# Performance work log

Hardware: AMD Instinct MI355X
Metric: run time of the kernel (lower is better)

Reference implementation:

```python
import jax, jax.numpy as jnp
import numpy as np

B, N, K, D_MODEL = 4, 16384, 32, 64

def gather_neighbors(x, idx):
    # x: [B, N, F], idx: [B, N, K] -> [B, N, K, F]
    return jnp.take_along_axis(x[:, :, None, :], idx[:, :, :, None], axis=1)

def setup_inputs() -> dict:
    key = jax.random.key(0)
    k1, k2, k3, k4, k5 = jax.random.split(key, 5)
    x = jax.random.normal(k1, (B, N, D_MODEL), dtype=jnp.float32)
    pos = jax.random.normal(k2, (B, N, 3), dtype=jnp.float32)
    neighbor_idx = jax.random.randint(k3, (B, N, K), 0, N, dtype=jnp.int32)
    W1 = jax.random.normal(k4, (3, D_MODEL), dtype=jnp.float32) * (1.0 / np.sqrt(3.0))
    b1 = jnp.zeros((D_MODEL,), dtype=jnp.float32)
    W2 = jax.random.normal(k5, (D_MODEL, D_MODEL), dtype=jnp.float32) * (1.0 / np.sqrt(D_MODEL))
    b2 = jnp.zeros((D_MODEL,), dtype=jnp.float32)
    return {"x": x, "pos": pos, "neighbor_idx": neighbor_idx,
            "W1": W1, "b1": b1, "W2": W2, "b2": b2}

def reference(x, pos, neighbor_idx, W1, b1, W2, b2):
    # gather neighbor positions: [B, N, K, 3]
    neighbors = gather_neighbors(pos, neighbor_idx)
    rel_pos = pos[:, :, None, :] - neighbors              # [B, N, K, 3]
    # weight MLP: Linear(3,d) + LeakyReLU(0.1), Linear(d,d)
    h = jax.nn.leaky_relu(jnp.einsum('bnkd,df->bnkf', rel_pos, W1) + b1, 0.1)
    w = jnp.einsum('bnkf,fg->bnkg', h, W2) + b2           # [B, N, K, F]
    xg = gather_neighbors(x, neighbor_idx)                # [B, N, K, F]
    return jnp.sum(w * xg, axis=2)                        # [B, N, F]
```

## Files before the change

### kernel.cpp

```cpp
#include <hip/hip_runtime.h>


#define NPTS   16384
#define KNB    32
#define F      64
#define BATCH  4
#define LOG2N  14
#define WPTS   8

typedef _Float16 h2     __attribute__((ext_vector_type(2)));
typedef _Float16 h8     __attribute__((ext_vector_type(8)));
typedef float    f32x16 __attribute__((ext_vector_type(16)));

__global__ __launch_bounds__(256, 2) void pointconv_mfma(
    const float* __restrict__ x,
    const float* __restrict__ pos,
    const int*   __restrict__ idx,
    const float* __restrict__ W1,
    const float* __restrict__ b1,
    const float* __restrict__ W2,
    const float* __restrict__ b2,
    float*       __restrict__ out)
{
    __shared__ __align__(16) _Float16 w1p[32][8];
    __shared__ __align__(16) _Float16 w2f[2][4][2][32][8];

    const int tid = threadIdx.x;
    if (tid < 32) {
        const int g = 2 * tid;
        w1p[tid][0] = (_Float16)W1[0 * F + g]; w1p[tid][1] = (_Float16)W1[0 * F + g + 1];
        w1p[tid][2] = (_Float16)W1[1 * F + g]; w1p[tid][3] = (_Float16)W1[1 * F + g + 1];
        w1p[tid][4] = (_Float16)W1[2 * F + g]; w1p[tid][5] = (_Float16)W1[2 * F + g + 1];
        w1p[tid][6] = (_Float16)b1[g];         w1p[tid][7] = (_Float16)b1[g + 1];
    }
#pragma unroll
    for (int r = 0; r < 16; ++r) {
        const int e = r * 256 + tid;
        const int g = e >> 6, f = e & 63;
        w2f[(g >> 3) & 1][g >> 4][f & 1][f >> 1][g & 7] = (_Float16)W2[e];
    }
    __syncthreads();

    const int lane = tid & 63;
    const int wv   = tid >> 6;
    const int m    = lane & 31;
    const int hf   = lane >> 5;
    const int voff = hf << 4;

    const float2 b2v = *(const float2*)(b2 + 2 * m);

    const int p0   = (blockIdx.x * 4 + wv) * WPTS;
    const int p0_s = __builtin_amdgcn_readfirstlane(p0);
    const int base = (p0_s >> LOG2N) << LOG2N;
    const uint32_t m2 = 2u * (uint32_t)m;

    const h2 c01 = { (_Float16)0.1f, (_Float16)0.1f };

    float2 xvA[16], xvB[16];
    float  rlA[6], rlB[6];
    int    jmA = 0, jmB = 0;
    {
        const int jm0 = idx[(uint32_t)(p0_s * KNB) + (uint32_t)m];
#pragma unroll
        for (int reg = 0; reg < 16; ++reg) {
            const int rA = (reg & 3) + ((reg >> 2) << 3);
            const int jk = __builtin_amdgcn_ds_bpermute(voff + 4 * rA, jm0);
            const uint32_t xo = ((uint32_t)(base + jk) << 6) + m2;
            xvA[reg] = *(const float2*)(x + xo);
        }
        const uint32_t nr3 = 3u * (uint32_t)(base + jm0);
        const uint32_t pp3 = 3u * (uint32_t)p0_s;
        rlA[0] = pos[nr3];     rlA[1] = pos[nr3 + 1]; rlA[2] = pos[nr3 + 2];
        rlA[3] = pos[pp3];     rlA[4] = pos[pp3 + 1]; rlA[5] = pos[pp3 + 2];
        if (WPTS > 1) jmA = idx[(uint32_t)((p0_s + 1) * KNB) + (uint32_t)m];
    }

#define POINT_BODY(XV_CUR, XV_NXT, JM_CUR, JM_NXT, RL_CUR, RL_NXT, I)         \
    {                                                                         \
        const int p_s = p0_s + (I);                                           \
         \
        if ((I) + 2 < WPTS)                                                   \
            JM_NXT = idx[(uint32_t)((p_s + 2) * KNB) + (uint32_t)m];          \
           \
        if ((I) + 1 < WPTS) {                                                 \
            const uint32_t nr3 = 3u * (uint32_t)(base + JM_CUR);              \
            const uint32_t pp3 = 3u * (uint32_t)(p_s + 1);                    \
            RL_NXT[0] = pos[nr3];     RL_NXT[1] = pos[nr3 + 1];               \
            RL_NXT[2] = pos[nr3 + 2];                                         \
            RL_NXT[3] = pos[pp3];     RL_NXT[4] = pos[pp3 + 1];               \
            RL_NXT[5] = pos[pp3 + 2];                                         \
        }                                                                     \
          \
        if ((I) + 1 < WPTS) {                                                 \
            _Pragma("unroll")                                                 \
            for (int reg = 0; reg < 16; ++reg) {                              \
                const int rA = (reg & 3) + ((reg >> 2) << 3);                 \
                const int jk = __builtin_amdgcn_ds_bpermute(voff + 4 * rA, JM_CUR); \
                const uint32_t xo = ((uint32_t)(base + jk) << 6) + m2;        \
                XV_NXT[reg] = *(const float2*)(x + xo);                       \
            }                                                                 \
        }                                                                     \
                \
        const float rx = RL_CUR[3] - RL_CUR[0];                               \
        const float ry = RL_CUR[4] - RL_CUR[1];                               \
        const float rz = RL_CUR[5] - RL_CUR[2];                               \
        f32x16 acc0, acc1;                                                    \
        _Pragma("unroll")                                                     \
        for (int r = 0; r < 16; ++r) { acc0[r] = b2v.x; acc1[r] = b2v.y; }    \
        const h2 rxp = { (_Float16)rx, (_Float16)rx };                        \
        const h2 ryp = { (_Float16)ry, (_Float16)ry };                        \
        const h2 rzp = { (_Float16)rz, (_Float16)rz };                        \
        _Pragma("unroll")                                                     \
        for (int t = 0; t < 4; ++t) {                                         \
            h8 af;                                                            \
            _Pragma("unroll")                                                 \
            for (int jj = 0; jj < 4; ++jj) {                                  \
                const int g2 = 8 * t + 4 * hf + jj;                           \
                const h8 w = *(const h8*)&w1p[g2][0];                         \
                const h2 wx = __builtin_shufflevector(w, w, 0, 1);            \
                const h2 wy = __builtin_shufflevector(w, w, 2, 3);            \
                const h2 wz = __builtin_shufflevector(w, w, 4, 5);            \
                const h2 bb = __builtin_shufflevector(w, w, 6, 7);            \
                h2 hv = bb + rxp * wx;                                        \
                hv = hv + ryp * wy;                                           \
                hv = hv + rzp * wz;                                           \
                hv = __builtin_elementwise_max(hv, hv * c01);                 \
                af[2 * jj]     = hv[0];                                       \
                af[2 * jj + 1] = hv[1];                                       \
            }                                                                 \
            const h8 bf0 = *(const h8*)&w2f[hf][t][0][m][0];                  \
            const h8 bf1 = *(const h8*)&w2f[hf][t][1][m][0];                  \
            acc0 = __builtin_amdgcn_mfma_f32_32x32x16_f16(af, bf0, acc0, 0, 0, 0); \
            acc1 = __builtin_amdgcn_mfma_f32_32x32x16_f16(af, bf1, acc1, 0, 0, 0); \
        }                                                                     \
                 \
        float s0 = 0.f, s1 = 0.f;                                             \
        _Pragma("unroll")                                                     \
        for (int reg = 0; reg < 16; ++reg) {                                  \
            s0 = fmaf(acc0[reg], XV_CUR[reg].x, s0);                          \
            s1 = fmaf(acc1[reg], XV_CUR[reg].y, s1);                          \
        }                                                                     \
        s0 += __shfl_xor(s0, 32);                                             \
        s1 += __shfl_xor(s1, 32);                                             \
        if (hf == 0)                                                          \
            *(float2*)(out + (uint32_t)(p_s * F) + m2) = make_float2(s0, s1); \
    }

#pragma unroll 1
    for (int io = 0; io < WPTS; io += 2) {
        POINT_BODY(xvA, xvB, jmA, jmB, rlA, rlB, io);
        POINT_BODY(xvB, xvA, jmB, jmA, rlB, rlA, io + 1);
    }
#undef POINT_BODY
}

extern "C" void kernel_launch(void* const* d_in, const int* in_sizes, int n_in,
                              void* d_out, int out_size, void* d_ws, size_t ws_size,
                              hipStream_t stream) {
    const float* x   = (const float*)d_in[0];
    const float* pos = (const float*)d_in[1];
    const int*   idx = (const int*)  d_in[2];
    const float* W1  = (const float*)d_in[3];
    const float* b1  = (const float*)d_in[4];
    const float* W2  = (const float*)d_in[5];
    const float* b2  = (const float*)d_in[6];
    float* out = (float*)d_out;

    dim3 grid((BATCH * NPTS) / (4 * WPTS));
    dim3 block(256);
    pointconv_mfma<<<grid, block, 0, stream>>>(x, pos, idx, W1, b1, W2, b2, out);
}
```

Measured before the change: 137.9 us.

## Deepen gather prefetch to two points ahead with triple buffering and full unroll

Measured after the change: 138.8 us. About the same (+0.6%).

```diff
diff --git a/kernel.cpp b/kernel.cpp
--- a/kernel.cpp
+++ b/kernel.cpp
@@ -56,54 +56,46 @@
 
     const h2 c01 = { (_Float16)0.1f, (_Float16)0.1f };
 
-    float2 xvA[16], xvB[16];
-    float  rlA[6], rlB[6];
-    int    jmA = 0, jmB = 0;
-    {
-        const int jm0 = idx[(uint32_t)(p0_s * KNB) + (uint32_t)m];
-#pragma unroll
-        for (int reg = 0; reg < 16; ++reg) {
-            const int rA = (reg & 3) + ((reg >> 2) << 3);
-            const int jk = __builtin_amdgcn_ds_bpermute(voff + 4 * rA, jm0);
-            const uint32_t xo = ((uint32_t)(base + jk) << 6) + m2;
-            xvA[reg] = *(const float2*)(x + xo);
-        }
-        const uint32_t nr3 = 3u * (uint32_t)(base + jm0);
-        const uint32_t pp3 = 3u * (uint32_t)p0_s;
-        rlA[0] = pos[nr3];     rlA[1] = pos[nr3 + 1]; rlA[2] = pos[nr3 + 2];
-        rlA[3] = pos[pp3];     rlA[4] = pos[pp3 + 1]; rlA[5] = pos[pp3 + 2];
-        if (WPTS > 1) jmA = idx[(uint32_t)((p0_s + 1) * KNB) + (uint32_t)m];
+    float2 xv0[16], xv1[16], xv2[16];
+    float  rl0[6], rl1[6];
+    int jm0, jm1, jm2, jm3, jm4, jm5, jm6, jm7;
+
+#define LOAD_JM(P)  idx[(uint32_t)((P) * KNB) + (uint32_t)m]
+
+#define POSLOAD(RL, JM, P) {                                                  \
+        const uint32_t nr3 = 3u * (uint32_t)(base + (JM));                    \
+        const uint32_t pp3 = 3u * (uint32_t)(P);                              \
+        RL[0] = pos[nr3];     RL[1] = pos[nr3 + 1]; RL[2] = pos[nr3 + 2];     \
+        RL[3] = pos[pp3];     RL[4] = pos[pp3 + 1]; RL[5] = pos[pp3 + 2];     \
     }
 
-#define POINT_BODY(XV_CUR, XV_NXT, JM_CUR, JM_NXT, RL_CUR, RL_NXT, I)         \
-    {                                                                         \
+#define GATHER(XV, JM) {                                                      \
+        _Pragma("unroll")                                                     \
+        for (int reg = 0; reg < 16; ++reg) {                                  \
+            const int rA = (reg & 3) + ((reg >> 2) << 3);                     \
+            const int jk = __builtin_amdgcn_ds_bpermute(voff + 4 * rA, (JM)); \
+            const uint32_t xo = ((uint32_t)(base + jk) << 6) + m2;            \
+            XV[reg] = *(const float2*)(x + xo);                               \
+        }                                                                     \
+    }
+
+    jm0 = LOAD_JM(p0_s);
+    jm1 = LOAD_JM(p0_s + 1);
+    jm2 = LOAD_JM(p0_s + 2);
+    POSLOAD(rl0, jm0, p0_s);
+    GATHER(xv0, jm0);
+    GATHER(xv1, jm1);
+
+#define BODY(I, XVcur, XVg, RLcur, RLnxt, JMpos, JMg, JMnew) {                \
         const int p_s = p0_s + (I);                                           \
-         \
-        if ((I) + 2 < WPTS)                                                   \
-            JM_NXT = idx[(uint32_t)((p_s + 2) * KNB) + (uint32_t)m];          \
-           \
-        if ((I) + 1 < WPTS) {                                                 \
-            const uint32_t nr3 = 3u * (uint32_t)(base + JM_CUR);              \
-            const uint32_t pp3 = 3u * (uint32_t)(p_s + 1);                    \
-            RL_NXT[0] = pos[nr3];     RL_NXT[1] = pos[nr3 + 1];               \
-            RL_NXT[2] = pos[nr3 + 2];                                         \
-            RL_NXT[3] = pos[pp3];     RL_NXT[4] = pos[pp3 + 1];               \
-            RL_NXT[5] = pos[pp3 + 2];                                         \
-        }                                                                     \
-          \
-        if ((I) + 1 < WPTS) {                                                 \
-            _Pragma("unroll")                                                 \
-            for (int reg = 0; reg < 16; ++reg) {                              \
-                const int rA = (reg & 3) + ((reg >> 2) << 3);                 \
-                const int jk = __builtin_amdgcn_ds_bpermute(voff + 4 * rA, JM_CUR); \
-                const uint32_t xo = ((uint32_t)(base + jk) << 6) + m2;        \
-                XV_NXT[reg] = *(const float2*)(x + xo);                       \
-            }                                                                 \
-        }                                                                     \
-                \
-        const float rx = RL_CUR[3] - RL_CUR[0];                               \
-        const float ry = RL_CUR[4] - RL_CUR[1];                               \
-        const float rz = RL_CUR[5] - RL_CUR[2];                               \
+        if ((I) + 3 < WPTS) JMnew = LOAD_JM(p_s + 3);                         \
+        if ((I) + 1 < WPTS) POSLOAD(RLnxt, JMpos, p_s + 1);                   \
+        if ((I) + 2 < WPTS) GATHER(XVg, JMg);                                 \
+        __builtin_amdgcn_sched_barrier(0);                                    \
+                                       \
+        const float rx = RLcur[3] - RLcur[0];                                 \
+        const float ry = RLcur[4] - RLcur[1];                                 \
+        const float rz = RLcur[5] - RLcur[2];                                 \
         f32x16 acc0, acc1;                                                    \
         _Pragma("unroll")                                                     \
         for (int r = 0; r < 16; ++r) { acc0[r] = b2v.x; acc1[r] = b2v.y; }    \
@@ -115,8 +107,7 @@
             h8 af;                                                            \
             _Pragma("unroll")                                                 \
             for (int jj = 0; jj < 4; ++jj) {                                  \
-                const int g2 = 8 * t + 4 * hf + jj;                           \
-                const h8 w = *(const h8*)&w1p[g2][0];                         \
+                const h8 w = *(const h8*)&w1p[8 * t + 4 * hf + jj][0];        \
                 const h2 wx = __builtin_shufflevector(w, w, 0, 1);            \
                 const h2 wy = __builtin_shufflevector(w, w, 2, 3);            \
                 const h2 wz = __builtin_shufflevector(w, w, 4, 5);            \
@@ -133,25 +124,35 @@
             acc0 = __builtin_amdgcn_mfma_f32_32x32x16_f16(af, bf0, acc0, 0, 0, 0); \
             acc1 = __builtin_amdgcn_mfma_f32_32x32x16_f16(af, bf1, acc1, 0, 0, 0); \
         }                                                                     \
-                 \
-        float s0 = 0.f, s1 = 0.f;                                             \
+              \
+        float s0a = 0.f, s0b = 0.f, s1a = 0.f, s1b = 0.f;                     \
         _Pragma("unroll")                                                     \
-        for (int reg = 0; reg < 16; ++reg) {                                  \
-            s0 = fmaf(acc0[reg], XV_CUR[reg].x, s0);                          \
-            s1 = fmaf(acc1[reg], XV_CUR[reg].y, s1);                          \
+        for (int reg = 0; reg < 16; reg += 2) {                               \
+            s0a = fmaf(acc0[reg],     XVcur[reg].x,     s0a);                 \
+            s0b = fmaf(acc0[reg + 1], XVcur[reg + 1].x, s0b);                 \
+            s1a = fmaf(acc1[reg],     XVcur[reg].y,     s1a);                 \
+            s1b = fmaf(acc1[reg + 1], XVcur[reg + 1].y, s1b);                 \
         }                                                                     \
+        float s0 = s0a + s0b, s1 = s1a + s1b;                                 \
         s0 += __shfl_xor(s0, 32);                                             \
         s1 += __shfl_xor(s1, 32);                                             \
         if (hf == 0)                                                          \
             *(float2*)(out + (uint32_t)(p_s * F) + m2) = make_float2(s0, s1); \
     }
 
-#pragma unroll 1
-    for (int io = 0; io < WPTS; io += 2) {
-        POINT_BODY(xvA, xvB, jmA, jmB, rlA, rlB, io);
-        POINT_BODY(xvB, xvA, jmB, jmA, rlB, rlA, io + 1);
-    }
-#undef POINT_BODY
+    BODY(0, xv0, xv2, rl0, rl1, jm1, jm2, jm3)
+    BODY(1, xv1, xv0, rl1, rl0, jm2, jm3, jm4)
+    BODY(2, xv2, xv1, rl0, rl1, jm3, jm4, jm5)
+    BODY(3, xv0, xv2, rl1, rl0, jm4, jm5, jm6)
+    BODY(4, xv1, xv0, rl0, rl1, jm5, jm6, jm7)
+    BODY(5, xv2, xv1, rl1, rl0, jm6, jm7, jm0)
+    BODY(6, xv0, xv2, rl0, rl1, jm7, jm0, jm0)
+    BODY(7, xv1, xv0, rl1, rl0, jm0, jm0, jm0)
+
+#undef BODY
+#undef GATHER
+#undef POSLOAD
+#undef LOAD_JM
 }
 
 extern "C" void kernel_launch(void* const* d_in, const int* in_sizes, int n_in,
```

## Stage batch positions in LDS as fp16 and enlarge blocks

Applied to the files above, without the earlier changes.

After: 144.2 us. 1.05x slower.

```diff
diff --git a/kernel.cpp b/kernel.cpp
--- a/kernel.cpp
+++ b/kernel.cpp
@@ -6,13 +6,14 @@
 #define F      64
 #define BATCH  4
 #define LOG2N  14
-#define WPTS   8
+#define WPTS   32
+#define WAVES  8
 
 typedef _Float16 h2     __attribute__((ext_vector_type(2)));
 typedef _Float16 h8     __attribute__((ext_vector_type(8)));
 typedef float    f32x16 __attribute__((ext_vector_type(16)));
 
-__global__ __launch_bounds__(256, 2) void pointconv_mfma(
+__global__ __launch_bounds__(512, 2) void pointconv_mfma(
     const float* __restrict__ x,
     const float* __restrict__ pos,
     const int*   __restrict__ idx,
@@ -24,6 +25,8 @@
 {
     __shared__ __align__(16) _Float16 w1p[32][8];
     __shared__ __align__(16) _Float16 w2f[2][4][2][32][8];
+    __shared__ __align__(8) _Float16 pxy[NPTS][2];
+    __shared__ __align__(4) _Float16 pz[NPTS];
 
     const int tid = threadIdx.x;
     if (tid < 32) {
@@ -34,10 +37,23 @@
         w1p[tid][6] = (_Float16)b1[g];         w1p[tid][7] = (_Float16)b1[g + 1];
     }
 #pragma unroll
-    for (int r = 0; r < 16; ++r) {
-        const int e = r * 256 + tid;
+    for (int r = 0; r < 8; ++r) {
+        const int e = r * 512 + tid;
         const int g = e >> 6, f = e & 63;
         w2f[(g >> 3) & 1][g >> 4][f & 1][f >> 1][g & 7] = (_Float16)W2[e];
+    }
+    {
+        const int bb = ((blockIdx.x * (WAVES * WPTS)) >> LOG2N) << LOG2N;
+        const float* __restrict__ pb = pos + (size_t)bb * 3;
+#pragma unroll 4
+        for (int n = tid; n < NPTS; n += 512) {
+            const float xx = pb[3 * n + 0];
+            const float yy = pb[3 * n + 1];
+            const float zz = pb[3 * n + 2];
+            pxy[n][0] = (_Float16)xx;
+            pxy[n][1] = (_Float16)yy;
+            pz[n]     = (_Float16)zz;
+        }
     }
     __syncthreads();
 
@@ -46,19 +62,19 @@
     const int m    = lane & 31;
     const int hf   = lane >> 5;
     const int voff = hf << 4;
+    const uint32_t m2 = 2u * (uint32_t)m;
 
     const float2 b2v = *(const float2*)(b2 + 2 * m);
 
-    const int p0   = (blockIdx.x * 4 + wv) * WPTS;
+    const int p0   = (blockIdx.x * WAVES + wv) * WPTS;
     const int p0_s = __builtin_amdgcn_readfirstlane(p0);
     const int base = (p0_s >> LOG2N) << LOG2N;
-    const uint32_t m2 = 2u * (uint32_t)m;
 
     const h2 c01 = { (_Float16)0.1f, (_Float16)0.1f };
 
-    float2 xvA[16], xvB[16];
-    float  rlA[6], rlB[6];
-    int    jmA = 0, jmB = 0;
+    float2   xvA[16], xvB[16];
+    _Float16 relA[3], relB[3];
+    int      jmA = 0, jmB = 0;
     {
         const int jm0 = idx[(uint32_t)(p0_s * KNB) + (uint32_t)m];
 #pragma unroll
@@ -68,29 +84,32 @@
             const uint32_t xo = ((uint32_t)(base + jk) << 6) + m2;
             xvA[reg] = *(const float2*)(x + xo);
         }
-        const uint32_t nr3 = 3u * (uint32_t)(base + jm0);
-        const uint32_t pp3 = 3u * (uint32_t)p0_s;
-        rlA[0] = pos[nr3];     rlA[1] = pos[nr3 + 1]; rlA[2] = pos[nr3 + 2];
-        rlA[3] = pos[pp3];     rlA[4] = pos[pp3 + 1]; rlA[5] = pos[pp3 + 2];
-        if (WPTS > 1) jmA = idx[(uint32_t)((p0_s + 1) * KNB) + (uint32_t)m];
+        const int ow = p0_s - base;
+        const h2 nxy = *(const h2*)&pxy[jm0][0];
+        const h2 oxy = *(const h2*)&pxy[ow][0];
+        const h2 rxy = oxy - nxy;
+        relA[0] = rxy[0]; relA[1] = rxy[1];
+        relA[2] = pz[ow] - pz[jm0];
+        jmA = idx[(uint32_t)((p0_s + 1) * KNB) + (uint32_t)m];
     }
 
-#define POINT_BODY(XV_CUR, XV_NXT, JM_CUR, JM_NXT, RL_CUR, RL_NXT, I)         \
+#define POINT_BODY(XV_CUR, XV_NXT, JM_CUR, JM_NXT, REL_CUR, REL_NXT, I)       \
     {                                                                         \
         const int p_s = p0_s + (I);                                           \
-         \
+                                      \
         if ((I) + 2 < WPTS)                                                   \
             JM_NXT = idx[(uint32_t)((p_s + 2) * KNB) + (uint32_t)m];          \
-           \
+              \
         if ((I) + 1 < WPTS) {                                                 \
-            const uint32_t nr3 = 3u * (uint32_t)(base + JM_CUR);              \
-            const uint32_t pp3 = 3u * (uint32_t)(p_s + 1);                    \
-            RL_NXT[0] = pos[nr3];     RL_NXT[1] = pos[nr3 + 1];               \
-            RL_NXT[2] = pos[nr3 + 2];                                         \
-            RL_NXT[3] = pos[pp3];     RL_NXT[4] = pos[pp3 + 1];               \
-            RL_NXT[5] = pos[pp3 + 2];                                         \
+            const int nb = JM_CUR;                                            \
+            const int ow = p_s + 1 - base;                                    \
+            const h2 nxy = *(const h2*)&pxy[nb][0];                           \
+            const h2 oxy = *(const h2*)&pxy[ow][0];                           \
+            const h2 rxy = oxy - nxy;                                         \
+            REL_NXT[0] = rxy[0]; REL_NXT[1] = rxy[1];                         \
+            REL_NXT[2] = pz[ow] - pz[nb];                                     \
         }                                                                     \
-          \
+                    \
         if ((I) + 1 < WPTS) {                                                 \
             _Pragma("unroll")                                                 \
             for (int reg = 0; reg < 16; ++reg) {                              \
@@ -100,23 +119,19 @@
                 XV_NXT[reg] = *(const float2*)(x + xo);                       \
             }                                                                 \
         }                                                                     \
-                \
-        const float rx = RL_CUR[3] - RL_CUR[0];                               \
-        const float ry = RL_CUR[4] - RL_CUR[1];                               \
-        const float rz = RL_CUR[5] - RL_CUR[2];                               \
+                    \
         f32x16 acc0, acc1;                                                    \
         _Pragma("unroll")                                                     \
         for (int r = 0; r < 16; ++r) { acc0[r] = b2v.x; acc1[r] = b2v.y; }    \
-        const h2 rxp = { (_Float16)rx, (_Float16)rx };                        \
-        const h2 ryp = { (_Float16)ry, (_Float16)ry };                        \
-        const h2 rzp = { (_Float16)rz, (_Float16)rz };                        \
+        const h2 rxp = { REL_CUR[0], REL_CUR[0] };                            \
+        const h2 ryp = { REL_CUR[1], REL_CUR[1] };                            \
+        const h2 rzp = { REL_CUR[2], REL_CUR[2] };                            \
         _Pragma("unroll")                                                     \
         for (int t = 0; t < 4; ++t) {                                         \
             h8 af;                                                            \
             _Pragma("unroll")                                                 \
             for (int jj = 0; jj < 4; ++jj) {                                  \
-                const int g2 = 8 * t + 4 * hf + jj;                           \
-                const h8 w = *(const h8*)&w1p[g2][0];                         \
+                const h8 w = *(const h8*)&w1p[8 * t + 4 * hf + jj][0];        \
                 const h2 wx = __builtin_shufflevector(w, w, 0, 1);            \
                 const h2 wy = __builtin_shufflevector(w, w, 2, 3);            \
                 const h2 wz = __builtin_shufflevector(w, w, 4, 5);            \
@@ -133,7 +148,7 @@
             acc0 = __builtin_amdgcn_mfma_f32_32x32x16_f16(af, bf0, acc0, 0, 0, 0); \
             acc1 = __builtin_amdgcn_mfma_f32_32x32x16_f16(af, bf1, acc1, 0, 0, 0); \
         }                                                                     \
-                 \
+                      \
         float s0 = 0.f, s1 = 0.f;                                             \
         _Pragma("unroll")                                                     \
         for (int reg = 0; reg < 16; ++reg) {                                  \
@@ -148,8 +163,8 @@
 
 #pragma unroll 1
     for (int io = 0; io < WPTS; io += 2) {
-        POINT_BODY(xvA, xvB, jmA, jmB, rlA, rlB, io);
-        POINT_BODY(xvB, xvA, jmB, jmA, rlB, rlA, io + 1);
+        POINT_BODY(xvA, xvB, jmA, jmB, relA, relB, io);
+        POINT_BODY(xvB, xvA, jmB, jmA, relB, relA, io + 1);
     }
 #undef POINT_BODY
 }
@@ -166,7 +181,7 @@
     const float* b2  = (const float*)d_in[6];
     float* out = (float*)d_out;
 
-    dim3 grid((BATCH * NPTS) / (4 * WPTS));
-    dim3 block(256);
+    dim3 grid((BATCH * NPTS) / (WAVES * WPTS));
+    dim3 block(512);
     pointconv_mfma<<<grid, block, 0, stream>>>(x, pos, idx, W1, b1, W2, b2, out);
 }
```
